# Performance work log

Measured on AMD Instinct MI355X. Metric: run time of the kernel, lower is better.

The kernel has to match this reference:

```python
import jax, jax.numpy as jnp
import numpy as np

N_SAMPLES = 32768
N_EVENTS = 16
WINDOW = 512
STEP = 256
N_FRAMES = 128          # n_samples // step_size
TOTAL_COEFFS = 16385    # n_samples // 2 + 1
N_COEFFS = 257          # window_size // 2 + 1
MIN_RES = 0.01


def max_norm(x):
    return x / (jnp.max(jnp.abs(x), axis=-1, keepdims=True) + 1e-8)


def linear_interp_last(x, out_size):
    """torch F.interpolate(mode='linear', align_corners=False) along last dim."""
    L = x.shape[-1]
    scale = L / out_size
    pos = (jnp.arange(out_size, dtype=jnp.float32) + 0.5) * scale - 0.5
    pos = jnp.clip(pos, 0.0, L - 1.0)
    i0 = jnp.floor(pos).astype(jnp.int32)
    i1 = jnp.minimum(i0 + 1, L - 1)
    w = pos - i0.astype(jnp.float32)
    return x[..., i0] * (1.0 - w) + x[..., i1] * w


def setup_inputs() -> dict:
    key = jax.random.key(0)
    k1, k2 = jax.random.split(key)
    x = jax.random.uniform(k1, (32, N_EVENTS, 533), dtype=jnp.float32)
    noise = jax.random.uniform(k2, (32, N_EVENTS, N_SAMPLES), dtype=jnp.float32)
    return {"x": x, "noise": noise}


def _forward(x, noise):
    x = jnp.clip(x, 0.0, 1.0)  # unit_activation

    # unpack
    means = x[..., 0:1] * 2.0 - 1.0                       # [B,E,1]
    stds = x[..., 1:2] * 0.1                              # [B,E,1]
    amps = x[..., 2:3]                                    # [B,E,1]
    res_mag = MIN_RES + (1.0 - MIN_RES) * x[..., 3:260]   # [B,E,257]
    freqs = (jnp.fft.rfftfreq(WINDOW) * np.pi).astype(jnp.float32)
    res_phase = x[..., 260:517] * (2.0 * np.pi) - np.pi + freqs  # [B,E,257]
    noise_coeff = x[..., 517:533]                         # [B,E,16]

    # ---- localized_noise ----
    rng = jnp.arange(N_SAMPLES, dtype=jnp.float32)
    mu = jnp.clip(means * N_SAMPLES, -(N_SAMPLES // 2), N_SAMPLES * 1.5)
    sigma = jnp.clip((1e-8 + stds) * N_SAMPLES, 0.0, N_SAMPLES - 1.0)
    logp = -0.5 * ((rng - mu) / sigma) ** 2 - jnp.log(sigma) - 0.5 * np.log(2.0 * np.pi)
    probs = max_norm(jnp.exp(logp))                       # [B,E,N]

    u = noise * 2.0 - 1.0                                 # uniform(-1,1)
    spec_shape = linear_interp_last(noise_coeff, TOTAL_COEFFS)  # [B,E,16385]
    nspec = jnp.fft.rfft(u, norm='ortho') * spec_shape
    nband = jnp.fft.irfft(nspec, n=N_SAMPLES, norm='ortho')
    atoms = probs * nband * amps                          # [B,E,N]

    # ---- resonance ----
    padded = jnp.pad(atoms, ((0, 0), (0, 0), (0, STEP)))
    idx = jnp.arange(N_FRAMES)[:, None] * STEP + jnp.arange(WINDOW)[None, :]
    frames = padded[..., idx]                             # [B,E,F,W]
    n = jnp.arange(WINDOW, dtype=jnp.float32)
    hamming = 0.54 - 0.46 * jnp.cos(2.0 * np.pi * n / WINDOW)  # periodic
    spec = jnp.fft.rfft(frames * hamming, norm='ortho')   # [B,E,F,257]

    # to_mag_and_phase
    re, im = spec.real, spec.imag
    mag = jnp.sqrt(re * re + im * im) + 1e-8              # [B,E,F,257]
    phase = (im / mag) * np.pi

    # mag recurrence m_t = mag_t + r * m_{t-1} (m_0 = mag_0) via scan over frames
    mag_t = jnp.moveaxis(mag, 2, 0)                       # [F,B,E,C]
    def step(carry, a):
        m = a + res_mag * carry
        return m, m
    _, ms = jax.lax.scan(step, jnp.zeros_like(mag_t[0]), mag_t)
    mags = jnp.moveaxis(ms, 0, 2)                         # [B,E,F,C]

    # phase: frame 0 unchanged, frames>=1 get + res_phase offset
    fmask = (jnp.arange(N_FRAMES) > 0).astype(phase.dtype)[None, None, :, None]
    phases = phase + fmask * res_phase[:, :, None, :]

    final = jax.lax.complex(mags * jnp.cos(phases), mags * jnp.sin(phases))
    res = jnp.fft.irfft(final, n=WINDOW, norm='ortho')    # [B,E,F,W]

    # overlap-add (hop = W/2), no window
    firsts, seconds = res[..., :STEP], res[..., STEP:]
    out = jnp.zeros(res.shape[:2] + (N_FRAMES + 1, STEP), res.dtype)
    out = out.at[:, :, :N_FRAMES].add(firsts).at[:, :, 1:].add(seconds)
    sig = out.reshape(out.shape[0], out.shape[1], -1)[..., :N_SAMPLES]  # [B,E,N]

    summed = jnp.sum(sig, axis=1, keepdims=True)          # [B,1,N]
    return max_norm(summed)


def reference(x, noise):
    return _forward(x, noise)
```

## Files before the change

### kernel.cpp

```cpp
#include <hip/hip_runtime.h>
#include <math.h>

#define PI_F 3.14159265358979323846f

__device__ __forceinline__ float2 cadd(float2 a, float2 b){ return make_float2(a.x+b.x, a.y+b.y); }
__device__ __forceinline__ float2 csub(float2 a, float2 b){ return make_float2(a.x-b.x, a.y-b.y); }
__device__ __forceinline__ float2 cmul(float2 a, float2 b){ return make_float2(a.x*b.x - a.y*b.y, a.x*b.y + a.y*b.x); }
__device__ __forceinline__ float2 cscale(float2 a, float s){ return make_float2(a.x*s, a.y*s); }
__device__ __forceinline__ float2 cconj(float2 a){ return make_float2(a.x, -a.y); }
__device__ __forceinline__ float clip01(float v){ return fminf(fmaxf(v, 0.0f), 1.0f); }

__device__ __forceinline__ float uniformf(float v){
  return __int_as_float(__builtin_amdgcn_readfirstlane(__float_as_int(v)));
}

__device__ __forceinline__ int swz14(int p){ return p ^ (15 & ((p>>4) ^ (p>>8) ^ (p>>12))); }
__device__ __forceinline__ int swz8 (int p){ return p ^ ((p>>4) & 15); }

__device__ __forceinline__ int dr14(int k){
  unsigned x = __brev((unsigned)k) >> 18;
  return (int)(((x & 0x1555u) << 1) | ((x >> 1) & 0x1555u));
}
__device__ __forceinline__ int dr8(int k){
  unsigned x = __brev((unsigned)k) >> 24;
  return (int)(((x & 0x55u) << 1) | ((x >> 1) & 0x55u));
}

__device__ __forceinline__ void unpack_pair(float2 Zk, float2 Zm, float sn, float cs,
                                            float2& Uk, float2& Um) {
  float2 A  = make_float2(0.5f*(Zk.x+Zm.x), 0.5f*(Zk.y-Zm.y));
  float2 B  = make_float2(Zk.x-Zm.x, Zk.y+Zm.y);
  Uk = cadd(A, cmul(B, make_float2(-0.5f*sn, -0.5f*cs)));
  float2 Bm = make_float2(-B.x, B.y);
  Um = cadd(make_float2(A.x, -A.y), cmul(Bm, make_float2(-0.5f*sn, 0.5f*cs)));
}
__device__ __forceinline__ void repack_pair(float2 Vk, float2 Vm, float sn, float cs,
                                            float2& Wk, float2& Wm) {
  float2 P = make_float2(Vk.x+Vm.x, Vk.y-Vm.y);
  float2 Q = make_float2(Vk.x-Vm.x, Vk.y+Vm.y);
  Wk = cscale(cadd(P, cmul(Q, make_float2(-sn, cs))), 0.5f);
  float2 Qm = make_float2(-Q.x, Q.y);
  Wm = cscale(cadd(make_float2(P.x, -P.y), cmul(Qm, make_float2(-sn, -cs))), 0.5f);
}

__device__ __forceinline__ float sshape(int k, const float* ncs) {
  float pos = ((float)k + 0.5f) * (16.0f/16385.0f) - 0.5f;
  pos = fminf(fmaxf(pos, 0.0f), 15.0f);
  float fi = floorf(pos);
  int i0 = (int)fi;
  int i1 = min(i0 + 1, 15);
  float w = pos - fi;
  return ncs[i0]*(1.0f-w) + ncs[i1]*w;
}

#define LGKM() asm volatile("s_waitcnt lgkmcnt(0)" ::: "memory")

__device__ __forceinline__ void big_stage_fwd(float2* Cb, int u, int J, int lj) {
  int j = u & (J-1);
  int base = ((u >> lj) << (lj+2)) | j;
  float2 a0 = Cb[swz14(base)];
  float2 a1 = Cb[swz14(base+J)];
  float2 a2 = Cb[swz14(base+2*J)];
  float2 a3 = Cb[swz14(base+3*J)];
  float sn, cs; __sincosf((float)j * (-PI_F/(2.0f*(float)J)), &sn, &cs);
  float2 w1 = make_float2(cs, sn), w2 = cmul(w1,w1), w3 = cmul(w2,w1);
  float2 t0 = cadd(a0,a2), t1 = cadd(a1,a3), t2 = csub(a0,a2), t3 = csub(a1,a3);
  float2 mi = make_float2(t3.y, -t3.x);
  Cb[swz14(base)]     = cadd(t0,t1);
  Cb[swz14(base+J)]   = cmul(cadd(t2,mi), w1);
  Cb[swz14(base+2*J)] = cmul(csub(t0,t1), w2);
  Cb[swz14(base+3*J)] = cmul(csub(t2,mi), w3);
}
__device__ __forceinline__ void big_stage_inv(float2* Cb, int u, int J, int lj) {
  int j = u & (J-1);
  int base = ((u >> lj) << (lj+2)) | j;
  float sn, cs; __sincosf((float)j * (PI_F/(2.0f*(float)J)), &sn, &cs);
  float2 v1 = make_float2(cs, sn), v2 = cmul(v1,v1), v3 = cmul(v2,v1);
  float2 b0 = Cb[swz14(base)];
  float2 b1 = cmul(Cb[swz14(base+J)],   v1);
  float2 b2 = cmul(Cb[swz14(base+2*J)], v2);
  float2 b3 = cmul(Cb[swz14(base+3*J)], v3);
  float2 s02 = cadd(b0,b2), d02 = csub(b0,b2), s13 = cadd(b1,b3), d13 = csub(b1,b3);
  float2 id13 = make_float2(-d13.y, d13.x);
  Cb[swz14(base)]     = cadd(s02, s13);
  Cb[swz14(base+J)]   = cadd(d02, id13);
  Cb[swz14(base+2*J)] = csub(s02, s13);
  Cb[swz14(base+3*J)] = csub(d02, id13);
}

__device__ __forceinline__ void fr2_fwd_t(float2* rowA, float2* rowB, int l, int J, int lj,
                                          const float2* wtab) {
  int j = l & (J-1);
  int base = ((l >> lj) << (lj+2)) | j;
  int i0 = swz8(base), i1 = swz8(base+J), i2 = swz8(base+2*J), i3 = swz8(base+3*J);
  int idx = j << (6 - lj);
  float2 a0=rowA[i0], a1=rowA[i1], a2=rowA[i2], a3=rowA[i3];
  float2 b0=rowB[i0], b1=rowB[i1], b2=rowB[i2], b3=rowB[i3];
  float2 w1 = wtab[idx], w2 = wtab[2*idx], w3 = wtab[3*idx];
  {
    float2 t0=cadd(a0,a2), t1=cadd(a1,a3), t2=csub(a0,a2), t3=csub(a1,a3);
    float2 mi=make_float2(t3.y,-t3.x);
    rowA[i0]=cadd(t0,t1);          rowA[i1]=cmul(cadd(t2,mi),w1);
    rowA[i2]=cmul(csub(t0,t1),w2); rowA[i3]=cmul(csub(t2,mi),w3);
  }
  {
    float2 t0=cadd(b0,b2), t1=cadd(b1,b3), t2=csub(b0,b2), t3=csub(b1,b3);
    float2 mi=make_float2(t3.y,-t3.x);
    rowB[i0]=cadd(t0,t1);          rowB[i1]=cmul(cadd(t2,mi),w1);
    rowB[i2]=cmul(csub(t0,t1),w2); rowB[i3]=cmul(csub(t2,mi),w3);
  }
}
__device__ __forceinline__ void fr2_inv_t(float2* rowA, float2* rowB, int l, int J, int lj,
                                          const float2* wtab) {
  int j = l & (J-1);
  int base = ((l >> lj) << (lj+2)) | j;
  int i0 = swz8(base), i1 = swz8(base+J), i2 = swz8(base+2*J), i3 = swz8(base+3*J);
  int idx = j << (6 - lj);
  float2 a0=rowA[i0], a1=rowA[i1], a2=rowA[i2], a3=rowA[i3];
  float2 b0=rowB[i0], b1=rowB[i1], b2=rowB[i2], b3=rowB[i3];
  float2 v1 = cconj(wtab[idx]), v2 = cconj(wtab[2*idx]), v3 = cconj(wtab[3*idx]);
  {
    float2 c1=cmul(a1,v1), c2=cmul(a2,v2), c3=cmul(a3,v3);
    float2 s02=cadd(a0,c2), d02=csub(a0,c2), s13=cadd(c1,c3), d13=csub(c1,c3);
    float2 id13=make_float2(-d13.y,d13.x);
    rowA[i0]=cadd(s02,s13); rowA[i1]=cadd(d02,id13);
    rowA[i2]=csub(s02,s13); rowA[i3]=csub(d02,id13);
  }
  {
    float2 c1=cmul(b1,v1), c2=cmul(b2,v2), c3=cmul(b3,v3);
    float2 s02=cadd(b0,c2), d02=csub(b0,c2), s13=cadd(c1,c3), d13=csub(c1,c3);
    float2 id13=make_float2(-d13.y,d13.x);
    rowB[i0]=cadd(s02,s13); rowB[i1]=cadd(d02,id13);
    rowB[i2]=csub(s02,s13); rowB[i3]=csub(d02,id13);
  }
}

__device__ __forceinline__ void fr_stage_fwd(float2* row, int u, int J, int lj) {
  int j = u & (J-1);
  int base = ((u >> lj) << (lj+2)) | j;
  float2 a0 = row[swz8(base)];
  float2 a1 = row[swz8(base+J)];
  float2 a2 = row[swz8(base+2*J)];
  float2 a3 = row[swz8(base+3*J)];
  float sn, cs; __sincosf((float)j * (-PI_F/(2.0f*(float)J)), &sn, &cs);
  float2 w1 = make_float2(cs, sn), w2 = cmul(w1,w1), w3 = cmul(w2,w1);
  float2 t0 = cadd(a0,a2), t1 = cadd(a1,a3), t2 = csub(a0,a2), t3 = csub(a1,a3);
  float2 mi = make_float2(t3.y, -t3.x);
  row[swz8(base)]     = cadd(t0,t1);
  row[swz8(base+J)]   = cmul(cadd(t2,mi), w1);
  row[swz8(base+2*J)] = cmul(csub(t0,t1), w2);
  row[swz8(base+3*J)] = cmul(csub(t2,mi), w3);
}
__device__ __forceinline__ void fr_stage_inv(float2* row, int u, int J, int lj) {
  int j = u & (J-1);
  int base = ((u >> lj) << (lj+2)) | j;
  float sn, cs; __sincosf((float)j * (PI_F/(2.0f*(float)J)), &sn, &cs);
  float2 v1 = make_float2(cs, sn), v2 = cmul(v1,v1), v3 = cmul(v2,v1);
  float2 b0 = row[swz8(base)];
  float2 b1 = cmul(row[swz8(base+J)],   v1);
  float2 b2 = cmul(row[swz8(base+2*J)], v2);
  float2 b3 = cmul(row[swz8(base+3*J)], v3);
  float2 s02 = cadd(b0,b2), d02 = csub(b0,b2), s13 = cadd(b1,b3), d13 = csub(b1,b3);
  float2 id13 = make_float2(-d13.y, d13.x);
  row[swz8(base)]     = cadd(s02, s13);
  row[swz8(base+J)]   = cadd(d02, id13);
  row[swz8(base+2*J)] = csub(s02, s13);
  row[swz8(base+3*J)] = csub(d02, id13);
}

__global__ void __launch_bounds__(1024, 1)
atoms_zero(float* __restrict__ out) { out[blockIdx.x * 1024 + threadIdx.x] = 0.0f; }

__global__ void __launch_bounds__(1024, 4)
atoms_noise(const float* __restrict__ x, const float* __restrict__ noise,
            float2* __restrict__ nbout) {
  const int blk = blockIdx.x;
  const int t   = threadIdx.x;

  const float* xr = x + (size_t)blk * 533;
  const float* nr = noise + (size_t)blk * 32768;

  __shared__ float2 Cs[16384];
  __shared__ float  ncs[16];

  if (t < 16) ncs[t] = clip01(xr[517 + t]);

  {
    const float4* nr4 = (const float4*)nr;
    #pragma unroll
    for (int i2 = 0; i2 < 8; ++i2) {
      int m = t + (i2 << 10);
      float4 v4 = nr4[m];
      Cs[swz14(2*m)]   = make_float2(v4.x*2.0f-1.0f, v4.y*2.0f-1.0f);
      Cs[swz14(2*m+1)] = make_float2(v4.z*2.0f-1.0f, v4.w*2.0f-1.0f);
    }
  }
  __syncthreads();

  const int ub = ((t >> 6) << 8) + (t & 63);

  #pragma unroll
  for (int r = 0; r < 4; ++r) big_stage_fwd(Cs, ub + (r<<6), 4096, 12);
  __syncthreads();
  #pragma unroll
  for (int r = 0; r < 4; ++r) big_stage_fwd(Cs, ub + (r<<6), 1024, 10);
  __syncthreads();
  #pragma unroll
  for (int r = 0; r < 4; ++r) big_stage_fwd(Cs, ub + (r<<6), 256, 8);
  LGKM();
  #pragma unroll
  for (int r = 0; r < 4; ++r) big_stage_fwd(Cs, ub + (r<<6), 64, 6);
  LGKM();
  #pragma unroll
  for (int r = 0; r < 4; ++r) big_stage_fwd(Cs, ub + (r<<6), 16, 4);
  LGKM();
  #pragma unroll
  for (int r = 0; r < 4; ++r) big_stage_fwd(Cs, ub + (r<<6), 4, 2);
  LGKM();
  #pragma unroll
  for (int r = 0; r < 4; ++r) big_stage_fwd(Cs, ub + (r<<6), 1, 0);
  __syncthreads();

  {
    const float invM = 1.0f / 16384.0f;
    for (int k = t; k < 8192; k += 1024) {
      if (k == 0) {
        float2 Z0 = Cs[0];
        float U0 = Z0.x + Z0.y;
        float UM = Z0.x - Z0.y;
        float V0 = U0 * sshape(0, ncs) * invM;
        float VM = UM * sshape(16384, ncs) * invM;
        Cs[0] = make_float2(0.5f*(V0+VM), 0.5f*(V0-VM));
      } else {
        int pk = swz14(dr14(k));
        int pm = swz14(dr14(16384 - k));
        float2 Zk = Cs[pk], Zm = Cs[pm];
        float sn, cs; __sincosf((float)k * (PI_F / 16384.0f), &sn, &cs);
        float2 Uk, Um; unpack_pair(Zk, Zm, sn, cs, Uk, Um);
        float2 Vk = cscale(Uk, sshape(k, ncs) * invM);
        float2 Vm = cscale(Um, sshape(16384 - k, ncs) * invM);
        float2 Wk, Wm; repack_pair(Vk, Vm, sn, cs, Wk, Wm);
        Cs[pk] = Wk; Cs[pm] = Wm;
      }
    }
    if (t == 0) {
      int p = swz14(2);
      float2 Z = Cs[p];
      float2 U = make_float2(Z.x, -Z.y);
      float2 V = cscale(U, sshape(8192, ncs) * invM);
      Cs[p] = make_float2(V.x, -V.y);
    }
  }
  __syncthreads();

  #pragma unroll
  for (int r = 0; r < 4; ++r) big_stage_inv(Cs, ub + (r<<6), 1, 0);
  LGKM();
  #pragma unroll
  for (int r = 0; r < 4; ++r) big_stage_inv(Cs, ub + (r<<6), 4, 2);
  LGKM();
  #pragma unroll
  for (int r = 0; r < 4; ++r) big_stage_inv(Cs, ub + (r<<6), 16, 4);
  LGKM();
  #pragma unroll
  for (int r = 0; r < 4; ++r) big_stage_inv(Cs, ub + (r<<6), 64, 6);
  LGKM();
  #pragma unroll
  for (int r = 0; r < 4; ++r) big_stage_inv(Cs, ub + (r<<6), 256, 8);
  __syncthreads();
  #pragma unroll
  for (int r = 0; r < 4; ++r) big_stage_inv(Cs, ub + (r<<6), 1024, 10);
  __syncthreads();
  #pragma unroll
  for (int r = 0; r < 4; ++r) big_stage_inv(Cs, ub + (r<<6), 4096, 12);
  __syncthreads();

  float2* dst = nbout + ((size_t)blk << 14);
  #pragma unroll
  for (int ii = 0; ii < 16; ++ii) {
    int j = t + (ii << 10);
    dst[j] = Cs[swz14(j)];
  }
}

__global__ void __launch_bounds__(512, 2)
atoms_frames(const float* __restrict__ x, const float2* __restrict__ nband,
             float2* __restrict__ wsrows) {
  const int blk = blockIdx.x;
  const int t   = threadIdx.x;
  const int w   = t >> 6;
  const int l   = t & 63;

  const float* xr = x + (size_t)blk * 533;
  const float2* nbd = nband + ((size_t)blk << 14);
  float2* wsrow = wsrows + ((size_t)blk << 14);

  __shared__ float2 FR[16][256];
  __shared__ float  magb[16*257];
  __shared__ float  phb[16*257];
  __shared__ float  resmag[257], resphase[257], msarr[257];
  __shared__ float2 carrybuf[2][128];
  __shared__ float2 hamtab[256];
  __shared__ float2 wtab[256];
  __shared__ float2 utab[129];

  const float xc0 = clip01(xr[0]);
  const float xc1 = clip01(xr[1]);
  const float amp = clip01(xr[2]);
  const float mean = xc0 * 2.0f - 1.0f;
  const float stdv = xc1 * 0.1f;
  float mu_v = fminf(fmaxf(mean * 32768.0f, -16384.0f), 49152.0f);
  float sigma = fminf(fmaxf((1e-8f + stdv) * 32768.0f, 0.0f), 32767.0f);
  float K_v = -logf(sigma) - 0.91893853320467274f;
  float invsig_v = 1.0f / sigma;
  float istar = fminf(fmaxf(roundf(mu_v), 0.0f), 32767.0f);
  float ds0 = (istar - mu_v) * invsig_v;
  float emax = __expf(-0.5f * ds0 * ds0 + K_v);
  const float mu     = uniformf(mu_v);
  const float invsig = uniformf(invsig_v);
  const float K      = uniformf(K_v);
  const float gscale = uniformf(amp / (emax + 1e-8f));

  if (t < 257) {
    resmag[t]   = 0.01f + 0.99f * clip01(xr[3 + t]);
    resphase[t] = clip01(xr[260 + t]) * (2.0f*PI_F) - PI_F + (float)t * (PI_F / 512.0f);
    msarr[t]    = 0.0f;
  }
  if (t < 128) carrybuf[0][t] = make_float2(0.0f, 0.0f);
  if (t < 256) {
    const float W512 = 2.0f * PI_F / 512.0f;
    float n0 = (float)(2*t);
    hamtab[t] = make_float2(0.54f - 0.46f*__cosf(n0*W512),
                            0.54f - 0.46f*__cosf((n0+1.0f)*W512));
    float s, c; __sincosf((float)t * (2.0f*PI_F/256.0f), &s, &c);
    wtab[t] = make_float2(c, -s);
  }
  if (t < 129) {
    float s, c; __sincosf((float)t * (PI_F/256.0f), &s, &c);
    utab[t] = make_float2(c, s);
  }
  __syncthreads();

  const float2 hm0 = hamtab[l];
  const float2 hm1 = hamtab[l + 64];
  const float2 hm2 = hamtab[l + 128];
  const float2 hm3 = hamtab[l + 192];

  const float C2 = 0.044194173824159216f;
  const float F2 = 0.08838834764831845f;
  const int iA = 2*w, iB = 2*w + 1;
  float2* rowA = FR[iA];
  float2* rowB = FR[iB];

  for (int g = 0; g < 8; ++g) {
    const int fgA = (g << 4) + iA;
    const int fgB = fgA + 1;

    #pragma unroll
    for (int s = 0; s < 2; ++s) {
      float2* row = s ? rowB : rowA;
      const int base = (s ? fgB : fgA) << 7;
      float2 a0 = make_float2(0.f,0.f), a1 = a0, a2 = a0, a3 = a0;
      {
        int c0 = base + l;
        if (c0 < 16384) {
          float2 nb = nbd[c0];
          float s0 = (float)(2*c0);
          float d0 = (s0 - mu) * invsig, d1 = (s0 + 1.0f - mu) * invsig;
          a0 = make_float2(__expf(-0.5f*d0*d0 + K)*gscale*nb.x*hm0.x,
                           __expf(-0.5f*d1*d1 + K)*gscale*nb.y*hm0.y);
        }
        int c1 = base + l + 64;
        if (c1 < 16384) {
          float2 nb = nbd[c1];
          float s0 = (float)(2*c1);
          float d0 = (s0 - mu) * invsig, d1 = (s0 + 1.0f - mu) * invsig;
          a1 = make_float2(__expf(-0.5f*d0*d0 + K)*gscale*nb.x*hm1.x,
                           __expf(-0.5f*d1*d1 + K)*gscale*nb.y*hm1.y);
        }
        int c2 = base + l + 128;
        if (c2 < 16384) {
          float2 nb = nbd[c2];
          float s0 = (float)(2*c2);
          float d0 = (s0 - mu) * invsig, d1 = (s0 + 1.0f - mu) * invsig;
          a2 = make_float2(__expf(-0.5f*d0*d0 + K)*gscale*nb.x*hm2.x,
                           __expf(-0.5f*d1*d1 + K)*gscale*nb.y*hm2.y);
        }
        int c3 = base + l + 192;
        if (c3 < 16384) {
          float2 nb = nbd[c3];
          float s0 = (float)(2*c3);
          float d0 = (s0 - mu) * invsig, d1 = (s0 + 1.0f - mu) * invsig;
          a3 = make_float2(__expf(-0.5f*d0*d0 + K)*gscale*nb.x*hm3.x,
                           __expf(-0.5f*d1*d1 + K)*gscale*nb.y*hm3.y);
        }
      }
      float2 w1 = wtab[l], w2 = wtab[2*l], w3 = wtab[(3*l) & 255];
      float2 t0 = cadd(a0,a2), t1 = cadd(a1,a3), t2 = csub(a0,a2), t3 = csub(a1,a3);
      float2 mi = make_float2(t3.y, -t3.x);
      row[swz8(l)]       = cadd(t0,t1);
      row[swz8(l+64)]    = cmul(cadd(t2,mi), w1);
      row[swz8(l+128)]   = cmul(csub(t0,t1), w2);
      row[swz8(l+192)]   = cmul(csub(t2,mi), w3);
    }
    LGKM();

    fr2_fwd_t(rowA, rowB, l, 16, 4, wtab); LGKM();
    fr2_fwd_t(rowA, rowB, l, 4, 2, wtab);  LGKM();
    fr2_fwd_t(rowA, rowB, l, 1, 0, wtab);  LGKM();

    if (l == 0) {
      #pragma unroll
      for (int s = 0; s < 2; ++s) {
        float2* row = s ? rowB : rowA;
        int ii = s ? iB : iA;
        float2 Z0 = row[0];
        float U0 = Z0.x + Z0.y, UM = Z0.x - Z0.y;
        magb[ii*257 + 0]   = fabsf(U0)*C2 + 1e-8f;
        magb[ii*257 + 256] = fabsf(UM)*C2 + 1e-8f;
        float2 Z = row[swz8(2)];
        float2 U = make_float2(Z.x, -Z.y);
        float mC = sqrtf(U.x*U.x + U.y*U.y)*C2 + 1e-8f;
        magb[ii*257 + 128] = mC;
        phb[ii*257 + 128]  = (U.y*C2/mC)*PI_F;
      }
    } else {
      int pk = swz8(dr8(l)), pm = swz8(dr8(256 - l));
      float2 uc = utab[l];
      #pragma unroll
      for (int s = 0; s < 2; ++s) {
        float2* row = s ? rowB : rowA;
        int ii = s ? iB : iA;
        float2 Uk, Um; unpack_pair(row[pk], row[pm], uc.y, uc.x, Uk, Um);
        float mk = sqrtf(Uk.x*Uk.x + Uk.y*Uk.y)*C2 + 1e-8f;
        float mm = sqrtf(Um.x*Um.x + Um.y*Um.y)*C2 + 1e-8f;
        magb[ii*257 + l]     = mk;
        magb[ii*257 + 256-l] = mm;
        phb[ii*257 + l]      = (Uk.y*C2/mk)*PI_F;
        phb[ii*257 + 256-l]  = (Um.y*C2/mm)*PI_F;
      }
    }
    {
      const int kB = l + 64;
      int pk = swz8(dr8(kB)), pm = swz8(dr8(256 - kB));
      float2 uc = utab[kB];
      #pragma unroll
      for (int s = 0; s < 2; ++s) {
        float2* row = s ? rowB : rowA;
        int ii = s ? iB : iA;
        float2 Uk, Um; unpack_pair(row[pk], row[pm], uc.y, uc.x, Uk, Um);
        float mk = sqrtf(Uk.x*Uk.x + Uk.y*Uk.y)*C2 + 1e-8f;
        float mm = sqrtf(Um.x*Um.x + Um.y*Um.y)*C2 + 1e-8f;
        magb[ii*257 + kB]     = mk;
        magb[ii*257 + 256-kB] = mm;
        phb[ii*257 + kB]      = (Uk.y*C2/mk)*PI_F;
        phb[ii*257 + 256-kB]  = (Um.y*C2/mm)*PI_F;
      }
    }
    __syncthreads();

    if (t < 257) {
      float rm = resmag[t], r = msarr[t];
      float mg[16];
      #pragma unroll
      for (int i = 0; i < 16; ++i) mg[i] = magb[i*257 + t];
      #pragma unroll
      for (int i = 0; i < 16; ++i) {
        r = fmaf(rm, r, mg[i]);
        magb[i*257 + t] = r;
      }
      msarr[t] = r;
    }
    __syncthreads();

    {
      const float fmA = (fgA > 0) ? 1.0f : 0.0f;
      if (l == 0) {
        #pragma unroll
        for (int s = 0; s < 2; ++s) {
          float2* row = s ? rowB : rowA;
          int ii = s ? iB : iA;
          float fm = s ? 1.0f : fmA;
          float ms0 = magb[ii*257 + 0]   * F2;
          float msM = magb[ii*257 + 256] * F2;
          float V0 = ms0 * __cosf(fm*resphase[0]);
          float VM = msM * __cosf(fm*resphase[256]);
          row[0] = make_float2(0.5f*(V0+VM), 0.5f*(V0-VM));
          float msC = magb[ii*257 + 128] * F2;
          float pC  = phb[ii*257 + 128] + fm*resphase[128];
          float sC, cC; __sincosf(pC, &sC, &cC);
          row[swz8(2)] = make_float2(msC*cC, -(msC*sC));
        }
      } else {
        int pk = swz8(dr8(l)), pm = swz8(dr8(256 - l));
        float2 uc = utab[l];
        float rp1 = resphase[l], rp2 = resphase[256-l];
        #pragma unroll
        for (int s = 0; s < 2; ++s) {
          float2* row = s ? rowB : rowA;
          int ii = s ? iB : iA;
          float fm = s ? 1.0f : fmA;
          float msk = magb[ii*257 + l]     * F2;
          float msm = magb[ii*257 + 256-l] * F2;
          float p1 = phb[ii*257 + l]     + fm*rp1;
          float p2 = phb[ii*257 + 256-l] + fm*rp2;
          float s1,c1,s2,c2; __sincosf(p1,&s1,&c1); __sincosf(p2,&s2,&c2);
          float2 Vk = make_float2(msk*c1, msk*s1);
          float2 Vm = make_float2(msm*c2, msm*s2);
          float2 Wk, Wm; repack_pair(Vk, Vm, uc.y, uc.x, Wk, Wm);
          row[pk] = Wk; row[pm] = Wm;
        }
      }
      {
        const int kB = l + 64;
        int pk = swz8(dr8(kB)), pm = swz8(dr8(256 - kB));
        float2 uc = utab[kB];
        float rp1 = resphase[kB], rp2 = resphase[256-kB];
        #pragma unroll
        for (int s = 0; s < 2; ++s) {
          float2* row = s ? rowB : rowA;
          int ii = s ? iB : iA;
          float fm = s ? 1.0f : fmA;
          float msk = magb[ii*257 + kB]     * F2;
          float msm = magb[ii*257 + 256-kB] * F2;
          float p1 = phb[ii*257 + kB]     + fm*rp1;
          float p2 = phb[ii*257 + 256-kB] + fm*rp2;
          float s1,c1,s2,c2; __sincosf(p1,&s1,&c1); __sincosf(p2,&s2,&c2);
          float2 Vk = make_float2(msk*c1, msk*s1);
          float2 Vm = make_float2(msm*c2, msm*s2);
          float2 Wk, Wm; repack_pair(Vk, Vm, uc.y, uc.x, Wk, Wm);
          row[pk] = Wk; row[pm] = Wm;
        }
      }
      LGKM();
      fr2_inv_t(rowA, rowB, l, 1, 0, wtab);  LGKM();
      fr2_inv_t(rowA, rowB, l, 4, 2, wtab);  LGKM();
      fr2_inv_t(rowA, rowB, l, 16, 4, wtab); LGKM();
      fr2_inv_t(rowA, rowB, l, 64, 6, wtab);
    }
    __syncthreads();

    #pragma unroll
    for (int rep = 0; rep < 4; ++rep) {
      int slot = t + (rep << 9);
      int i = slot >> 7, j = slot & 127;
      int fg = (g << 4) + i;
      float2 first  = FR[i][swz8(j)];
      float2 second = (i > 0) ? FR[i-1][swz8(128 + j)] : carrybuf[g & 1][j];
      wsrow[(fg << 7) + j] = cadd(first, second);
      if (i == 15) {
        carrybuf[(g & 1) ^ 1][j] = FR[15][swz8(128 + j)];
      }
    }
    __syncthreads();
  }
}

__global__ void __launch_bounds__(1024, 4)
atoms_main(const float* __restrict__ x, const float* __restrict__ noise,
           float* __restrict__ outacc, float2* __restrict__ wsbuf, int use_ws) {
  const int blk = blockIdx.x;
  const int b   = blk >> 4;
  const int t   = threadIdx.x;
  const int w   = t >> 6;
  const int l   = t & 63;

  const float* xr = x + (size_t)blk * 533;
  const float* nr = noise + (size_t)blk * 32768;

  __shared__ float2 Cs[16384];
  __shared__ float2 FR[8][256];
  __shared__ float  magb[8*257];
  __shared__ float  resmag[257], resphase[257], msarr[257];
  __shared__ float2 carrybuf[2][128];
  __shared__ float2 hamtab[256];
  __shared__ float  ncs[16];

  const float xc0 = clip01(xr[0]);
  const float xc1 = clip01(xr[1]);
  const float amp = clip01(xr[2]);
  const float mean = xc0 * 2.0f - 1.0f;
  const float stdv = xc1 * 0.1f;
  float mu_v = fminf(fmaxf(mean * 32768.0f, -16384.0f), 49152.0f);
  float sigma = fminf(fmaxf((1e-8f + stdv) * 32768.0f, 0.0f), 32767.0f);
  float K_v = -logf(sigma) - 0.91893853320467274f;
  float invsig_v = 1.0f / sigma;
  float istar = fminf(fmaxf(roundf(mu_v), 0.0f), 32767.0f);
  float ds0 = (istar - mu_v) * invsig_v;
  float emax = __expf(-0.5f * ds0 * ds0 + K_v);
  const float mu     = uniformf(mu_v);
  const float invsig = uniformf(invsig_v);
  const float K      = uniformf(K_v);
  const float gscale = uniformf(amp / (emax + 1e-8f));

  if (t < 257) {
    resmag[t]   = 0.01f + 0.99f * clip01(xr[3 + t]);
    resphase[t] = clip01(xr[260 + t]) * (2.0f*PI_F) - PI_F + (float)t * (PI_F / 512.0f);
    msarr[t]    = 0.0f;
  }
  if (t < 16)  ncs[t] = clip01(xr[517 + t]);
  if (t < 128) carrybuf[0][t] = make_float2(0.0f, 0.0f);
  if (t < 256) {
    const float W512 = 2.0f * PI_F / 512.0f;
    float n0 = (float)(2*t);
    hamtab[t] = make_float2(0.54f - 0.46f*__cosf(n0*W512),
                            0.54f - 0.46f*__cosf((n0+1.0f)*W512));
  }

  {
    const float4* nr4 = (const float4*)nr;
    #pragma unroll
    for (int i2 = 0; i2 < 8; ++i2) {
      int m = t + (i2 << 10);
      float4 v4 = nr4[m];
      Cs[swz14(2*m)]   = make_float2(v4.x*2.0f-1.0f, v4.y*2.0f-1.0f);
      Cs[swz14(2*m+1)] = make_float2(v4.z*2.0f-1.0f, v4.w*2.0f-1.0f);
    }
  }
  __syncthreads();

  const int ub = ((t >> 6) << 8) + (t & 63);

  #pragma unroll
  for (int r = 0; r < 4; ++r) big_stage_fwd(Cs, ub + (r<<6), 4096, 12);
  __syncthreads();
  #pragma unroll
  for (int r = 0; r < 4; ++r) big_stage_fwd(Cs, ub + (r<<6), 1024, 10);
  __syncthreads();
  #pragma unroll
  for (int r = 0; r < 4; ++r) big_stage_fwd(Cs, ub + (r<<6), 256, 8);
  LGKM();
  #pragma unroll
  for (int r = 0; r < 4; ++r) big_stage_fwd(Cs, ub + (r<<6), 64, 6);
  LGKM();
  #pragma unroll
  for (int r = 0; r < 4; ++r) big_stage_fwd(Cs, ub + (r<<6), 16, 4);
  LGKM();
  #pragma unroll
  for (int r = 0; r < 4; ++r) big_stage_fwd(Cs, ub + (r<<6), 4, 2);
  LGKM();
  #pragma unroll
  for (int r = 0; r < 4; ++r) big_stage_fwd(Cs, ub + (r<<6), 1, 0);
  __syncthreads();

  {
    const float invM = 1.0f / 16384.0f;
    for (int k = t; k < 8192; k += 1024) {
      if (k == 0) {
        float2 Z0 = Cs[0];
        float U0 = Z0.x + Z0.y;
        float UM = Z0.x - Z0.y;
        float V0 = U0 * sshape(0, ncs) * invM;
        float VM = UM * sshape(16384, ncs) * invM;
        Cs[0] = make_float2(0.5f*(V0+VM), 0.5f*(V0-VM));
      } else {
        int pk = swz14(dr14(k));
        int pm = swz14(dr14(16384 - k));
        float2 Zk = Cs[pk], Zm = Cs[pm];
        float sn, cs; __sincosf((float)k * (PI_F / 16384.0f), &sn, &cs);
        float2 Uk, Um; unpack_pair(Zk, Zm, sn, cs, Uk, Um);
        float2 Vk = cscale(Uk, sshape(k, ncs) * invM);
        float2 Vm = cscale(Um, sshape(16384 - k, ncs) * invM);
        float2 Wk, Wm; repack_pair(Vk, Vm, sn, cs, Wk, Wm);
        Cs[pk] = Wk; Cs[pm] = Wm;
      }
    }
    if (t == 0) {
      int p = swz14(2);
      float2 Z = Cs[p];
      float2 U = make_float2(Z.x, -Z.y);
      float2 V = cscale(U, sshape(8192, ncs) * (1.0f/16384.0f));
      Cs[p] = make_float2(V.x, -V.y);
    }
  }
  __syncthreads();

  #pragma unroll
  for (int r = 0; r < 4; ++r) big_stage_inv(Cs, ub + (r<<6), 1, 0);
  LGKM();
  #pragma unroll
  for (int r = 0; r < 4; ++r) big_stage_inv(Cs, ub + (r<<6), 4, 2);
  LGKM();
  #pragma unroll
  for (int r = 0; r < 4; ++r) big_stage_inv(Cs, ub + (r<<6), 16, 4);
  LGKM();
  #pragma unroll
  for (int r = 0; r < 4; ++r) big_stage_inv(Cs, ub + (r<<6), 64, 6);
  LGKM();
  #pragma unroll
  for (int r = 0; r < 4; ++r) big_stage_inv(Cs, ub + (r<<6), 256, 8);
  __syncthreads();
  #pragma unroll
  for (int r = 0; r < 4; ++r) big_stage_inv(Cs, ub + (r<<6), 1024, 10);
  __syncthreads();
  #pragma unroll
  for (int r = 0; r < 4; ++r) big_stage_inv(Cs, ub + (r<<6), 4096, 12);
  __syncthreads();

  const float C2 = 0.044194173824159216f;
  const float F2 = 0.08838834764831845f;
  float2* row = (w < 8) ? FR[w] : FR[0];
  float2* wsrow = use_ws ? (wsbuf + ((size_t)blk << 14)) : (float2*)0;

  for (int g = 0; g < 16; ++g) {
    #pragma unroll
    for (int rep = 0; rep < 2; ++rep) {
      int slot = t + (rep << 10);
      int i = slot >> 8, j = slot & 255;
      int fg = (g << 3) + i;
      int cidx = (fg << 7) + j;
      float2 v = make_float2(0.0f, 0.0f);
      if (cidx < 16384) {
        float2 nb = Cs[swz14(cidx)];
        float s0 = (float)(2*cidx);
        float d0 = (s0 - mu) * invsig;
        float d1 = (s0 + 1.0f - mu) * invsig;
        float2 h = hamtab[j];
        v = make_float2(__expf(-0.5f*d0*d0 + K) * gscale * nb.x * h.x,
                        __expf(-0.5f*d1*d1 + K) * gscale * nb.y * h.y);
      }
      FR[i][swz8(j)] = v;
    }
    __syncthreads();

    if (w < 8) {
      fr_stage_fwd(row, l, 64, 6); LGKM();
      fr_stage_fwd(row, l, 16, 4); LGKM();
      fr_stage_fwd(row, l, 4, 2);  LGKM();
      fr_stage_fwd(row, l, 1, 0);  LGKM();

      if (l == 0) {
        float2 Z0 = row[0];
        float U0 = Z0.x + Z0.y, UM = Z0.x - Z0.y;
        magb[w*257 + 0]   = fabsf(U0)*C2 + 1e-8f;
        magb[w*257 + 256] = fabsf(UM)*C2 + 1e-8f;
        float2 Z = row[swz8(2)];
        magb[w*257 + 128] = sqrtf(Z.x*Z.x + Z.y*Z.y)*C2 + 1e-8f;
      } else {
        int pk = swz8(dr8(l)), pm = swz8(dr8(256 - l));
        float sn, cs; __sincosf((float)l * (PI_F/256.0f), &sn, &cs);
        float2 Uk, Um; unpack_pair(row[pk], row[pm], sn, cs, Uk, Um);
        magb[w*257 + l]     = sqrtf(Uk.x*Uk.x + Uk.y*Uk.y)*C2 + 1e-8f;
        magb[w*257 + 256-l] = sqrtf(Um.x*Um.x + Um.y*Um.y)*C2 + 1e-8f;
      }
      {
        const int kB = l + 64;
        int pk = swz8(dr8(kB)), pm = swz8(dr8(256 - kB));
        float sn, cs; __sincosf((float)kB * (PI_F/256.0f), &sn, &cs);
        float2 Uk, Um; unpack_pair(row[pk], row[pm], sn, cs, Uk, Um);
        magb[w*257 + kB]     = sqrtf(Uk.x*Uk.x + Uk.y*Uk.y)*C2 + 1e-8f;
        magb[w*257 + 256-kB] = sqrtf(Um.x*Um.x + Um.y*Um.y)*C2 + 1e-8f;
      }
    }
    __syncthreads();

    if (t < 257) {
      float rm = resmag[t], r = msarr[t];
      #pragma unroll
      for (int i = 0; i < 8; ++i) {
        float mg = magb[i*257 + t];
        r = fmaf(rm, r, mg);
        magb[i*257 + t] = r;
      }
      msarr[t] = r;
    }
    __syncthreads();

    if (w < 8) {
      float fm = ((g << 3) + w > 0) ? 1.0f : 0.0f;
      if (l == 0) {
        float ms0 = magb[w*257 + 0]   * F2;
        float msM = magb[w*257 + 256] * F2;
        float V0 = ms0 * __cosf(fm*resphase[0]);
        float VM = msM * __cosf(fm*resphase[256]);
        row[0] = make_float2(0.5f*(V0+VM), 0.5f*(V0-VM));
        float2 Z = row[swz8(2)];
        float2 U = make_float2(Z.x, -Z.y);
        float mC = sqrtf(U.x*U.x + U.y*U.y)*C2 + 1e-8f;
        float pC = (U.y*C2/mC)*PI_F + fm*resphase[128];
        float msC = magb[w*257 + 128] * F2;
        float sC, cC; __sincosf(pC, &sC, &cC);
        row[swz8(2)] = make_float2(msC*cC, -(msC*sC));
      } else {
        int pk = swz8(dr8(l)), pm = swz8(dr8(256 - l));
        float sn, cs; __sincosf((float)l * (PI_F/256.0f), &sn, &cs);
        float2 Uk, Um; unpack_pair(row[pk], row[pm], sn, cs, Uk, Um);
        float mk = sqrtf(Uk.x*Uk.x + Uk.y*Uk.y)*C2 + 1e-8f;
        float mm = sqrtf(Um.x*Um.x + Um.y*Um.y)*C2 + 1e-8f;
        float p1 = (Uk.y*C2/mk)*PI_F + fm*resphase[l];
        float p2 = (Um.y*C2/mm)*PI_F + fm*resphase[256-l];
        float msk = magb[w*257 + l]     * F2;
        float msm = magb[w*257 + 256-l] * F2;
        float s1,c1,s2,c2; __sincosf(p1,&s1,&c1); __sincosf(p2,&s2,&c2);
        float2 Vk = make_float2(msk*c1, msk*s1);
        float2 Vm = make_float2(msm*c2, msm*s2);
        float2 Wk, Wm; repack_pair(Vk, Vm, sn, cs, Wk, Wm);
        row[pk] = Wk; row[pm] = Wm;
      }
      {
        const int kB = l + 64;
        int pk = swz8(dr8(kB)), pm = swz8(dr8(256 - kB));
        float sn, cs; __sincosf((float)kB * (PI_F/256.0f), &sn, &cs);
        float2 Uk, Um; unpack_pair(row[pk], row[pm], sn, cs, Uk, Um);
        float mk = sqrtf(Uk.x*Uk.x + Uk.y*Uk.y)*C2 + 1e-8f;
        float mm = sqrtf(Um.x*Um.x + Um.y*Um.y)*C2 + 1e-8f;
        float p1 = (Uk.y*C2/mk)*PI_F + fm*resphase[kB];
        float p2 = (Um.y*C2/mm)*PI_F + fm*resphase[256-kB];
        float msk = magb[w*257 + kB]     * F2;
        float msm = magb[w*257 + 256-kB] * F2;
        float s1,c1,s2,c2; __sincosf(p1,&s1,&c1); __sincosf(p2,&s2,&c2);
        float2 Vk = make_float2(msk*c1, msk*s1);
        float2 Vm = make_float2(msm*c2, msm*s2);
        float2 Wk, Wm; repack_pair(Vk, Vm, sn, cs, Wk, Wm);
        row[pk] = Wk; row[pm] = Wm;
      }
      LGKM();
      fr_stage_inv(row, l, 1, 0);  LGKM();
      fr_stage_inv(row, l, 4, 2);  LGKM();
      fr_stage_inv(row, l, 16, 4); LGKM();
      fr_stage_inv(row, l, 64, 6);
    }
    __syncthreads();

    {
      int i = t >> 7, j = t & 127;
      int fg = (g << 3) + i;
      float2 first  = FR[i][swz8(j)];
      float2 second = (i > 0) ? FR[i-1][swz8(128 + j)] : carrybuf[g & 1][j];
      float2 v = cadd(first, second);
      if (use_ws) {
        wsrow[(fg << 7) + j] = v;
      } else {
        float* dst = outacc + (size_t)b*32768 + (fg << 8) + 2*j;
        atomicAdd(dst,     v.x);
        atomicAdd(dst + 1, v.y);
      }
      if (i == 7) {
        carrybuf[(g & 1) ^ 1][j] = FR[7][swz8(128 + j)];
      }
    }
    __syncthreads();
  }
}

__global__ void __launch_bounds__(1024, 1)
atoms_sum_max(const float* __restrict__ ws, float* __restrict__ out, float* __restrict__ wmax) {
  int blk = blockIdx.x;
  int b = blk >> 3, seg = blk & 7, tid = threadIdx.x;
  const float* base = ws + (size_t)b*16*32768 + (size_t)seg*4096;
  float v[4]; float m = 0.0f;
  #pragma unroll
  for (int i = 0; i < 4; ++i) {
    int idx = (i << 10) + tid;
    float s = 0.0f;
    #pragma unroll
    for (int e = 0; e < 16; ++e) s += base[(size_t)e*32768 + idx];
    v[i] = s; m = fmaxf(m, fabsf(s));
  }
  float* op = out + (size_t)b*32768 + (seg << 12);
  #pragma unroll
  for (int i = 0; i < 4; ++i) op[(i<<10) + tid] = v[i];
  __shared__ float red[1024];
  red[tid] = m; __syncthreads();
  for (int s2 = 512; s2 > 0; s2 >>= 1) {
    if (tid < s2) red[tid] = fmaxf(red[tid], red[tid + s2]);
    __syncthreads();
  }
  if (tid == 0) wmax[blk] = red[0];
}

__global__ void __launch_bounds__(1024, 1)
atoms_scale(float* __restrict__ out, const float* __restrict__ wmax) {
  int blk = blockIdx.x;
  int b = blk >> 3, seg = blk & 7, tid = threadIdx.x;
  const float* wm = wmax + b*8;
  float m = fmaxf(fmaxf(fmaxf(wm[0],wm[1]), fmaxf(wm[2],wm[3])),
                  fmaxf(fmaxf(wm[4],wm[5]), fmaxf(wm[6],wm[7])));
  float inv = 1.0f / (m + 1e-8f);
  float* op = out + (size_t)b*32768 + (seg << 12);
  #pragma unroll
  for (int i = 0; i < 4; ++i) op[(i<<10) + tid] *= inv;
}

__global__ void __launch_bounds__(1024, 1)
atoms_norm(float* __restrict__ out) {
  const int b = blockIdx.x;
  const int tid = threadIdx.x;
  float* p = out + (size_t)b * 32768;
  __shared__ float red[1024];
  float m = 0.0f;
  for (int i = tid; i < 32768; i += 1024) m = fmaxf(m, fabsf(p[i]));
  red[tid] = m;
  __syncthreads();
  for (int s = 512; s > 0; s >>= 1) {
    if (tid < s) red[tid] = fmaxf(red[tid], red[tid + s]);
    __syncthreads();
  }
  const float inv = 1.0f / (red[0] + 1e-8f);
  for (int i = tid; i < 32768; i += 1024) p[i] = p[i] * inv;
}

extern "C" void kernel_launch(void* const* d_in, const int* in_sizes, int n_in,
                              void* d_out, int out_size, void* d_ws, size_t ws_size,
                              hipStream_t stream) {
  (void)in_sizes; (void)n_in; (void)out_size;
  const float* x     = (const float*)d_in[0];
  const float* noise = (const float*)d_in[1];
  float* out = (float*)d_out;

  const size_t rows_f    = 512ull * 32768ull;
  const size_t need_ws    = rows_f*4 + 4096;
  const size_t need_split = rows_f*4 + 4096 + rows_f*4;

  if (d_ws != nullptr && ws_size >= need_split) {
    float* ws    = (float*)d_ws;
    float* wmax  = ws + rows_f;
    float2* nbd  = (float2*)(ws + rows_f + 1024);
    atoms_noise <<<512, 1024, 0, stream>>>(x, noise, nbd);
    atoms_frames<<<512,  512, 0, stream>>>(x, nbd, (float2*)ws);
    atoms_sum_max<<<256, 1024, 0, stream>>>(ws, out, wmax);
    atoms_scale<<<256, 1024, 0, stream>>>(out, wmax);
  } else if (d_ws != nullptr && ws_size >= need_ws) {
    float* ws = (float*)d_ws;
    float* wmax = ws + rows_f;
    atoms_main<<<512, 1024, 0, stream>>>(x, noise, nullptr, (float2*)ws, 1);
    atoms_sum_max<<<256, 1024, 0, stream>>>(ws, out, wmax);
    atoms_scale<<<256, 1024, 0, stream>>>(out, wmax);
  } else {
    atoms_zero<<<1024, 1024, 0, stream>>>(out);
    atoms_main<<<512, 1024, 0, stream>>>(x, noise, out, nullptr, 0);
    atoms_norm<<<32, 1024, 0, stream>>>(out);
  }
}
```

Before: 246.7 us.

## Pack magnitude/phase as fp16 pairs in LDS and drop shared lookup tables

Replaces the separate fp32 magnitude and phase LDS buffers with one packed half2-style word per coefficient. It also removes the hamming, resmag, resphase and msarr shared tables, computing those values into registers per thread instead. The goal is to cut LDS footprint, which may allow more resident blocks, and to reduce LDS traffic in the scan and repack stages. The cost is fp16 rounding of magnitudes in the recurrence scan and of phases, which risks accuracy. It also adds register pressure and extra per-thread cos work.

Result: no change. 248.9 us (+0.9%).

```diff
diff --git a/kernel.cpp b/kernel.cpp
--- a/kernel.cpp
+++ b/kernel.cpp
@@ -1,4 +1,5 @@
 #include <hip/hip_runtime.h>
+#include <hip/hip_fp16.h>
 #include <math.h>
 
 #define PI_F 3.14159265358979323846f
@@ -12,6 +13,17 @@
 
 __device__ __forceinline__ float uniformf(float v){
   return __int_as_float(__builtin_amdgcn_readfirstlane(__float_as_int(v)));
+}
+
+__device__ __forceinline__ unsigned packmp(float mg, float ph){
+  return ((unsigned)__half_as_ushort(__float2half_rn(ph)) << 16) |
+          (unsigned)__half_as_ushort(__float2half_rn(mg));
+}
+__device__ __forceinline__ float mp_mag(unsigned u){
+  return __half2float(__ushort_as_half((unsigned short)(u & 0xFFFFu)));
+}
+__device__ __forceinline__ float mp_ph(unsigned u){
+  return __half2float(__ushort_as_half((unsigned short)(u >> 16)));
 }
 
 __device__ __forceinline__ int swz14(int p){ return p ^ (15 & ((p>>4) ^ (p>>8) ^ (p>>12))); }
@@ -295,14 +307,11 @@
   const float2* nbd = nband + ((size_t)blk << 14);
   float2* wsrow = wsrows + ((size_t)blk << 14);
 
-  __shared__ float2 FR[16][256];
-  __shared__ float  magb[16*257];
-  __shared__ float  phb[16*257];
-  __shared__ float  resmag[257], resphase[257], msarr[257];
-  __shared__ float2 carrybuf[2][128];
-  __shared__ float2 hamtab[256];
-  __shared__ float2 wtab[256];
-  __shared__ float2 utab[129];
+  __shared__ float2   FR[16][256];
+  __shared__ unsigned magph[16*257];
+  __shared__ float2   carrybuf[2][128];
+  __shared__ float2   wtab[192];
+  __shared__ float2   utab[128];
 
   const float xc0 = clip01(xr[0]);
   const float xc1 = clip01(xr[1]);
@@ -321,30 +330,34 @@
   const float K      = uniformf(K_v);
   const float gscale = uniformf(amp / (emax + 1e-8f));
 
-  if (t < 257) {
-    resmag[t]   = 0.01f + 0.99f * clip01(xr[3 + t]);
-    resphase[t] = clip01(xr[260 + t]) * (2.0f*PI_F) - PI_F + (float)t * (PI_F / 512.0f);
-    msarr[t]    = 0.0f;
-  }
-  if (t < 128) carrybuf[0][t] = make_float2(0.0f, 0.0f);
-  if (t < 256) {
-    const float W512 = 2.0f * PI_F / 512.0f;
-    float n0 = (float)(2*t);
-    hamtab[t] = make_float2(0.54f - 0.46f*__cosf(n0*W512),
-                            0.54f - 0.46f*__cosf((n0+1.0f)*W512));
+  if (t < 192) {
     float s, c; __sincosf((float)t * (2.0f*PI_F/256.0f), &s, &c);
     wtab[t] = make_float2(c, -s);
   }
-  if (t < 129) {
+  if (t < 128) {
     float s, c; __sincosf((float)t * (PI_F/256.0f), &s, &c);
     utab[t] = make_float2(c, s);
-  }
-  __syncthreads();
-
-  const float2 hm0 = hamtab[l];
-  const float2 hm1 = hamtab[l + 64];
-  const float2 hm2 = hamtab[l + 128];
-  const float2 hm3 = hamtab[l + 192];
+    carrybuf[0][t] = make_float2(0.0f, 0.0f);
+  }
+  __syncthreads();
+
+  const float W512 = 2.0f * PI_F / 512.0f;
+  #define HAMP(n) (0.54f - 0.46f*__cosf((float)(n)*W512))
+  const float2 hm0 = make_float2(HAMP(2*l),       HAMP(2*l+1));
+  const float2 hm1 = make_float2(HAMP(2*l+128),   HAMP(2*l+129));
+  const float2 hm2 = make_float2(HAMP(2*l+256),   HAMP(2*l+257));
+  const float2 hm3 = make_float2(HAMP(2*l+384),   HAMP(2*l+385));
+  #undef HAMP
+
+  #define RPH(k) (clip01(xr[260 + (k)]) * (2.0f*PI_F) - PI_F + (float)(k) * (PI_F/512.0f))
+  const float rp1 = RPH(l);
+  const float rp2 = RPH(256 - l);
+  const float rp3 = RPH(l + 64);
+  const float rp4 = RPH(192 - l);
+  const float rpC = RPH(128);
+  float scan_rm = 0.0f, scan_r = 0.0f;
+  if (t < 257) scan_rm = 0.01f + 0.99f * clip01(xr[3 + t]);
+  #undef RPH
 
   const float C2 = 0.044194173824159216f;
   const float F2 = 0.08838834764831845f;
@@ -395,7 +408,7 @@
                            __expf(-0.5f*d1*d1 + K)*gscale*nb.y*hm3.y);
         }
       }
-      float2 w1 = wtab[l], w2 = wtab[2*l], w3 = wtab[(3*l) & 255];
+      float2 w1 = wtab[l], w2 = wtab[2*l], w3 = wtab[3*l];
       float2 t0 = cadd(a0,a2), t1 = cadd(a1,a3), t2 = csub(a0,a2), t3 = csub(a1,a3);
       float2 mi = make_float2(t3.y, -t3.x);
       row[swz8(l)]       = cadd(t0,t1);
@@ -416,13 +429,12 @@
         int ii = s ? iB : iA;
         float2 Z0 = row[0];
         float U0 = Z0.x + Z0.y, UM = Z0.x - Z0.y;
-        magb[ii*257 + 0]   = fabsf(U0)*C2 + 1e-8f;
-        magb[ii*257 + 256] = fabsf(UM)*C2 + 1e-8f;
+        magph[ii*257 + 0]   = packmp(fabsf(U0)*C2 + 1e-8f, 0.0f);
+        magph[ii*257 + 256] = packmp(fabsf(UM)*C2 + 1e-8f, 0.0f);
         float2 Z = row[swz8(2)];
         float2 U = make_float2(Z.x, -Z.y);
         float mC = sqrtf(U.x*U.x + U.y*U.y)*C2 + 1e-8f;
-        magb[ii*257 + 128] = mC;
-        phb[ii*257 + 128]  = (U.y*C2/mC)*PI_F;
+        magph[ii*257 + 128] = packmp(mC, (U.y*C2/mC)*PI_F);
       }
     } else {
       int pk = swz8(dr8(l)), pm = swz8(dr8(256 - l));
@@ -434,10 +446,8 @@
         float2 Uk, Um; unpack_pair(row[pk], row[pm], uc.y, uc.x, Uk, Um);
         float mk = sqrtf(Uk.x*Uk.x + Uk.y*Uk.y)*C2 + 1e-8f;
         float mm = sqrtf(Um.x*Um.x + Um.y*Um.y)*C2 + 1e-8f;
-        magb[ii*257 + l]     = mk;
-        magb[ii*257 + 256-l] = mm;
-        phb[ii*257 + l]      = (Uk.y*C2/mk)*PI_F;
-        phb[ii*257 + 256-l]  = (Um.y*C2/mm)*PI_F;
+        magph[ii*257 + l]     = packmp(mk, (Uk.y*C2/mk)*PI_F);
+        magph[ii*257 + 256-l] = packmp(mm, (Um.y*C2/mm)*PI_F);
       }
     }
     {
@@ -451,25 +461,24 @@
         float2 Uk, Um; unpack_pair(row[pk], row[pm], uc.y, uc.x, Uk, Um);
         float mk = sqrtf(Uk.x*Uk.x + Uk.y*Uk.y)*C2 + 1e-8f;
         float mm = sqrtf(Um.x*Um.x + Um.y*Um.y)*C2 + 1e-8f;
-        magb[ii*257 + kB]     = mk;
-        magb[ii*257 + 256-kB] = mm;
-        phb[ii*257 + kB]      = (Uk.y*C2/mk)*PI_F;
-        phb[ii*257 + 256-kB]  = (Um.y*C2/mm)*PI_F;
+        magph[ii*257 + kB]     = packmp(mk, (Uk.y*C2/mk)*PI_F);
+        magph[ii*257 + 256-kB] = packmp(mm, (Um.y*C2/mm)*PI_F);
       }
     }
     __syncthreads();
 
     if (t < 257) {
-      float rm = resmag[t], r = msarr[t];
-      float mg[16];
+      unsigned uu[16];
       #pragma unroll
-      for (int i = 0; i < 16; ++i) mg[i] = magb[i*257 + t];
+      for (int i = 0; i < 16; ++i) uu[i] = magph[i*257 + t];
+      float r = scan_r;
       #pragma unroll
       for (int i = 0; i < 16; ++i) {
-        r = fmaf(rm, r, mg[i]);
-        magb[i*257 + t] = r;
-      }
-      msarr[t] = r;
+        r = fmaf(scan_rm, r, mp_mag(uu[i]));
+        magph[i*257 + t] = (uu[i] & 0xFFFF0000u) |
+                           (unsigned)__half_as_ushort(__float2half_rn(r));
+      }
+      scan_r = r;
     }
     __syncthreads();
 
@@ -481,29 +490,30 @@
           float2* row = s ? rowB : rowA;
           int ii = s ? iB : iA;
           float fm = s ? 1.0f : fmA;
-          float ms0 = magb[ii*257 + 0]   * F2;
-          float msM = magb[ii*257 + 256] * F2;
-          float V0 = ms0 * __cosf(fm*resphase[0]);
-          float VM = msM * __cosf(fm*resphase[256]);
+          float ms0 = mp_mag(magph[ii*257 + 0])   * F2;
+          float msM = mp_mag(magph[ii*257 + 256]) * F2;
+          float V0 = ms0 * __cosf(fm*rp1);
+          float VM = msM * __cosf(fm*rp2);
           row[0] = make_float2(0.5f*(V0+VM), 0.5f*(V0-VM));
-          float msC = magb[ii*257 + 128] * F2;
-          float pC  = phb[ii*257 + 128] + fm*resphase[128];
+          unsigned uC = magph[ii*257 + 128];
+          float msC = mp_mag(uC) * F2;
+          float pC  = mp_ph(uC) + fm*rpC;
           float sC, cC; __sincosf(pC, &sC, &cC);
           row[swz8(2)] = make_float2(msC*cC, -(msC*sC));
         }
       } else {
         int pk = swz8(dr8(l)), pm = swz8(dr8(256 - l));
         float2 uc = utab[l];
-        float rp1 = resphase[l], rp2 = resphase[256-l];
         #pragma unroll
         for (int s = 0; s < 2; ++s) {
           float2* row = s ? rowB : rowA;
           int ii = s ? iB : iA;
           float fm = s ? 1.0f : fmA;
-          float msk = magb[ii*257 + l]     * F2;
-          float msm = magb[ii*257 + 256-l] * F2;
-          float p1 = phb[ii*257 + l]     + fm*rp1;
-          float p2 = phb[ii*257 + 256-l] + fm*rp2;
+          unsigned uk = magph[ii*257 + l], um = magph[ii*257 + 256-l];
+          float msk = mp_mag(uk) * F2;
+          float msm = mp_mag(um) * F2;
+          float p1 = mp_ph(uk) + fm*rp1;
+          float p2 = mp_ph(um) + fm*rp2;
           float s1,c1,s2,c2; __sincosf(p1,&s1,&c1); __sincosf(p2,&s2,&c2);
           float2 Vk = make_float2(msk*c1, msk*s1);
           float2 Vm = make_float2(msm*c2, msm*s2);
@@ -515,16 +525,16 @@
         const int kB = l + 64;
         int pk = swz8(dr8(kB)), pm = swz8(dr8(256 - kB));
         float2 uc = utab[kB];
-        float rp1 = resphase[kB], rp2 = resphase[256-kB];
         #pragma unroll
         for (int s = 0; s < 2; ++s) {
           float2* row = s ? rowB : rowA;
           int ii = s ? iB : iA;
           float fm = s ? 1.0f : fmA;
-          float msk = magb[ii*257 + kB]     * F2;
-          float msm = magb[ii*257 + 256-kB] * F2;
-          float p1 = phb[ii*257 + kB]     + fm*rp1;
-          float p2 = phb[ii*257 + 256-kB] + fm*rp2;
+          unsigned uk = magph[ii*257 + kB], um = magph[ii*257 + 256-kB];
+          float msk = mp_mag(uk) * F2;
+          float msm = mp_mag(um) * F2;
+          float p1 = mp_ph(uk) + fm*rp3;
+          float p2 = mp_ph(um) + fm*rp4;
           float s1,c1,s2,c2; __sincosf(p1,&s1,&c1); __sincosf(p2,&s2,&c2);
           float2 Vk = make_float2(msk*c1, msk*s1);
           float2 Vm = make_float2(msm*c2, msm*s2);
```
